# Kernel optimization log

Hardware: AMD Instinct MI355X
Metric: run time of the kernel (lower is better)

## Reference

```python
import jax, jax.numpy as jnp
import numpy as np


def setup_inputs() -> dict:
    key = jax.random.key(0)
    k0, k1, k2, k3 = jax.random.split(key, 4)
    B, S, D, F, E = 8, 2048, 1024, 2048, 8
    x = jax.random.normal(k0, (B, S, D), dtype=jnp.float32)
    Wg = jax.random.normal(k1, (D, E), dtype=jnp.float32) * 0.02
    W1 = jax.random.normal(k2, (E, D, F), dtype=jnp.float32) * 0.02
    W2 = jax.random.normal(k3, (E, F, D), dtype=jnp.float32) * 0.02
    return {"x": x, "Wg": Wg, "W1": W1, "W2": W2}


def reference(x, Wg, W1, W2):
    # Expert-choice MoE: experts pick top-C tokens, conflicts resolved by
    # max router prob (ties -> lowest expert index, matching the serial loop).
    B, S, D = x.shape
    E = Wg.shape[1]
    T = B * S
    cap = max(1, T // E)  # capacity_factor = 1.0

    xt = x.reshape(T, D)
    logits = xt @ Wg                      # [T, E]
    probs = jax.nn.softmax(logits, axis=-1)
    pT = probs.T                          # [E, T] token affinities per expert

    _, top_idx = jax.lax.top_k(pT, cap)   # [E, cap] tokens chosen by each expert
    sel = jnp.zeros((E, T), dtype=bool).at[jnp.arange(E)[:, None], top_idx].set(True)

    # Serial conflict loop is equivalent to: per token, pick the selecting
    masked = jnp.where(sel, pT, -jnp.inf)
    assigned = sel.any(axis=0)            # [T]
    tok2exp = jnp.where(assigned,
                        jnp.argmax(masked, axis=0),
                        jnp.argmax(pT, axis=0))          # [T] int
    weights = jnp.take_along_axis(probs, tok2exp[:, None], axis=1)[:, 0]  # [T]

    # Dispatch / expert FFN / weighted combine. Loop over the small fixed
    # expert set; masked tokens contribute exactly zero, matching index_add_.
    out = jnp.zeros_like(xt)
    for e in range(E):
        gate = jnp.where(tok2exp == e, weights, 0.0)     # [T]
        h = jax.nn.gelu(xt @ W1[e], approximate=False) @ W2[e]  # [T, D]
        out = out + gate[:, None] * h

    return out.reshape(B, S, D)
```

## Files before the change

kernel.cpp:

```cpp
#include <hip/hip_runtime.h>
#include <hip/hip_bf16.h>
#include <math.h>

#define T_TOK 16384
#define DIM   1024
#define FF    2048
#define NE    8
#define CAPK  2048
#define WL1SZ 4096
#define WL2SZ 2048
#define NB_W2T 4096

typedef unsigned short u16;
typedef unsigned long long u64;
typedef __attribute__((ext_vector_type(8))) short bf16x8;
typedef __attribute__((ext_vector_type(4))) float f32x4;

__device__ __forceinline__ u16 f2bf(float f) {
  __hip_bfloat16 h = __float2bfloat16(f);
  union { __hip_bfloat16 h; u16 u; } c; c.h = h; return c.u;
}

__device__ __forceinline__ float gelu_f(float v) {
  float z = fabsf(v) * 0.70710678118654752f;
  float t = __builtin_amdgcn_rcpf(1.0f + 0.3275911f * z);
  float poly = t * (0.254829592f +
               t * (-0.284496736f +
               t * (1.421413741f +
               t * (-1.453152027f +
               t * 1.061405429f))));
  float ez = __expf(-z * z);
  float erfz = 1.0f - poly * ez;
  erfz = copysignf(erfz, v);
  return 0.5f * v * (1.0f + erfz);
}

__device__ __forceinline__ void async_copy16(const void* g, void* l) {
  __builtin_amdgcn_global_load_lds(
      (const __attribute__((address_space(1))) unsigned int*)g,
      (__attribute__((address_space(3))) unsigned int*)l, 16, 0, 0);
}

__device__ __forceinline__ bf16x8 ds_read16(const char* p) {
  bf16x8 r;
  asm volatile("ds_read_b128 %0, %1"
               : "=&v"(r)
               : "v"((const __attribute__((address_space(3))) char*)p));
  return r;
}

#define LGKM0()                                                                   \
  do {                                                                            \
    asm volatile("s_waitcnt lgkmcnt(0)" ::: "memory");                            \
    __builtin_amdgcn_sched_barrier(0);                                            \
  } while (0)
#define VMW0() asm volatile("s_waitcnt vmcnt(0)" ::: "memory")
#define VMW4() asm volatile("s_waitcnt vmcnt(4)" ::: "memory")
#define BAR() asm volatile("s_barrier" ::: "memory")

__device__ __forceinline__ void transpose_tile(const float* __restrict__ src,
                                               u16* __restrict__ dst, int R, int C,
                                               int bxy, int tid, float (*tile)[65]) {
  int nbx = C >> 6;
  int bx = bxy % nbx, by = bxy / nbx;
  int r0 = by * 64, c0 = bx * 64;
  int lr = tid >> 4, lc4 = (tid & 15) * 4;
#pragma unroll
  for (int p = 0; p < 4; ++p) {
    float4 v = *(const float4*)(src + (size_t)(r0 + p * 16 + lr) * C + c0 + lc4);
    tile[p * 16 + lr][lc4 + 0] = v.x;
    tile[p * 16 + lr][lc4 + 1] = v.y;
    tile[p * 16 + lr][lc4 + 2] = v.z;
    tile[p * 16 + lr][lc4 + 3] = v.w;
  }
  __syncthreads();
  int oc = tid >> 3, orr = (tid & 7) * 8;
#pragma unroll
  for (int p = 0; p < 2; ++p) {
    int c = p * 32 + oc;
    u16 h[8];
#pragma unroll
    for (int j = 0; j < 8; ++j) h[j] = f2bf(tile[orr + j][c]);
    *(uint4*)(dst + (size_t)(c0 + c) * R + r0 + orr) = *(uint4*)h;
  }
}

__global__ __launch_bounds__(256) void prep_k(const float* __restrict__ x,
                                              const float* __restrict__ Wg,
                                              const float* __restrict__ W1,
                                              float* __restrict__ probs,
                                              float* __restrict__ probsT,
                                              u16* __restrict__ xb,
                                              u16* __restrict__ w1t,
                                              u64* __restrict__ key,
                                              int* cnt, int* cnt2, int* gates) {
  __shared__ float tile[64][65];
  int bid = blockIdx.x, tid = threadIdx.x;
  if (bid < 4096) {
    if (tid < 4) key[bid * 4 + tid] = 0ull;
    if (bid == 0 && tid < NE) { cnt[tid] = 0; cnt2[tid] = 0; }
    if (bid == 0 && tid >= 8 && tid < 10) gates[tid - 8] = 0;
    int wid = tid >> 6, lane = tid & 63;
    int t = bid * 4 + wid;
    const float* xr = x + (size_t)t * DIM;
    u16* xbr = xb + (size_t)t * DIM;
    double acc[NE] = {0, 0, 0, 0, 0, 0, 0, 0};
#pragma unroll
    for (int it = 0; it < DIM / 64; ++it) {
      int d = it * 64 + lane;
      float xv = xr[d];
      xbr[d] = f2bf(xv);
      const float4* wrow = (const float4*)(Wg + (size_t)d * NE);
      float4 w0 = wrow[0], w1 = wrow[1];
      acc[0] += (double)xv * (double)w0.x;
      acc[1] += (double)xv * (double)w0.y;
      acc[2] += (double)xv * (double)w0.z;
      acc[3] += (double)xv * (double)w0.w;
      acc[4] += (double)xv * (double)w1.x;
      acc[5] += (double)xv * (double)w1.y;
      acc[6] += (double)xv * (double)w1.z;
      acc[7] += (double)xv * (double)w1.w;
    }
#pragma unroll
    for (int e = 0; e < NE; ++e)
      for (int o = 32; o > 0; o >>= 1) acc[e] += __shfl_down(acc[e], o, 64);
    if (lane == 0) {
      float l[NE], mx = -3.0e38f;
#pragma unroll
      for (int e = 0; e < NE; ++e) { l[e] = (float)acc[e]; mx = fmaxf(mx, l[e]); }
      float s = 0.f;
#pragma unroll
      for (int e = 0; e < NE; ++e) { l[e] = expf(l[e] - mx); s += l[e]; }
      float inv = 1.0f / s;
#pragma unroll
      for (int e = 0; e < NE; ++e) {
        float p = l[e] * inv;
        probs[(size_t)t * NE + e] = p;
        probsT[(size_t)e * T_TOK + t] = p;
      }
    }
  } else {
    int tz = bid - 4096;
    int z = tz >> 9, bxy = tz & 511;
    transpose_tile(W1 + (size_t)z * DIM * FF, w1t + (size_t)z * DIM * FF,
                   DIM, FF, bxy, tid, tile);
  }
}

__global__ __launch_bounds__(256) void moe_route_k(const float* __restrict__ probsT,
                                                   const float* __restrict__ probs,
                                                   const float* __restrict__ W2,
                                                   u16* __restrict__ w2t,
                                                   u64* __restrict__ key,
                                                   int* __restrict__ tok2exp,
                                                   float* __restrict__ wgt,
                                                   int* cnt, int* cnt2,
                                                   int* __restrict__ list,
                                                   int* basep, int* wl1, int* wl2,
                                                   int* gates) {
  __shared__ char shm[17472];
  int bid = blockIdx.x, tid = threadIdx.x, wid = tid >> 6, lane = tid & 63;
  if (bid < 8) {
    unsigned* whist = (unsigned*)shm;
    unsigned* hist  = (unsigned*)(shm + 16384);
    unsigned* bcast = (unsigned*)(shm + 17408);
    unsigned* wsum  = (unsigned*)(shm + 17424);
    int*      wps   = (int*)(shm + 17440);
    int e = bid;
    const float* pT = probsT + (size_t)e * T_TOK;
    unsigned prefix = 0, remaining = CAPK;
#pragma unroll 1
    for (int lvl = 0; lvl < 4; ++lvl) {
      int shift = 24 - 8 * lvl;
      unsigned cv;
      if (lvl == 0) {
        for (int i = tid; i < 16 * 256; i += 256) whist[i] = 0;
        __syncthreads();
        int sub = wid * 4 + (lane & 3);
        for (int i = tid; i < T_TOK; i += 256)
          atomicAdd(&whist[sub * 256 + (__float_as_uint(pT[i]) >> 24)], 1u);
        __syncthreads();
        cv = 0;
#pragma unroll
        for (int w = 0; w < 16; ++w) cv += whist[w * 256 + tid];
      } else {
        hist[tid] = 0;
        __syncthreads();
        for (int i = tid; i < T_TOK; i += 256) {
          unsigned k = __float_as_uint(pT[i]);
          if ((k >> (shift + 8)) == prefix)
            atomicAdd(&hist[(k >> shift) & 255u], 1u);
        }
        __syncthreads();
        cv = hist[tid];
      }
      unsigned s = cv;
#pragma unroll
      for (int o = 1; o < 64; o <<= 1) {
        unsigned tv = __shfl_down(s, o, 64);
        if (lane + o < 64) s += tv;
      }
      if (lane == 0) wsum[wid] = s;
      __syncthreads();
      unsigned above = 0;
      for (int w = wid + 1; w < 4; ++w) above += wsum[w];
      unsigned Sincl = s + above, Sexcl = Sincl - cv;
      if (Sincl >= remaining && Sexcl < remaining) {
        bcast[0] = (unsigned)tid;
        bcast[1] = remaining - Sexcl;
      }
      __syncthreads();
      prefix = (prefix << 8) | bcast[0];
      remaining = bcast[1];
      __syncthreads();
    }
    unsigned vk = prefix;
    int need = (int)remaining;
    const int CH = T_TOK / 256;
    int i0 = tid * CH;
    int myt = 0;
    for (int i = i0; i < i0 + CH; ++i)
      myt += (__float_as_uint(pT[i]) == vk);
    int p = myt;
#pragma unroll
    for (int o = 1; o < 64; o <<= 1) {
      int tv = __shfl_up(p, o, 64);
      if (lane >= o) p += tv;
    }
    if (lane == 63) wps[wid] = p;
    __syncthreads();
    int wo = 0;
    for (int w = 0; w < wid; ++w) wo += wps[w];
    int run = wo + p - myt;
    u64 ebits = (u64)(7 - e);
    for (int i = i0; i < i0 + CH; ++i) {
      unsigned k = __float_as_uint(pT[i]);
      bool sv = false;
      if (k > vk) sv = true;
      else if (k == vk) { if (run < need) sv = true; run++; }
      if (sv) atomicMax(&key[i], ((u64)k << 3) | ebits);
    }
    __threadfence();
    __syncthreads();
    if (tid == 0) atomicAdd(&gates[0], 1);
  } else if (bid < 72) {
    if (tid == 0) {
      while (atomicAdd(&gates[0], 0) < 8) __builtin_amdgcn_s_sleep(8);
    }
    __syncthreads();
    __threadfence();
    int gid = (bid - 8) * 256 + tid;
    u64 k = key[gid];
    int best;
    float bp;
    if (k) {
      best = 7 - (int)(k & 7);
      bp = __uint_as_float((unsigned)(k >> 3));
    } else {
      best = 0; bp = -3.0e38f;
#pragma unroll
      for (int e = 0; e < NE; ++e) {
        float p = probs[(size_t)gid * NE + e];
        if (p > bp) { bp = p; best = e; }
      }
    }
    tok2exp[gid] = best;
    wgt[gid] = bp;
#pragma unroll
    for (int e = 0; e < NE; ++e) {
      u64 m = __ballot(best == e);
      if (best == e && lane == __ffsll(m) - 1) atomicAdd(&cnt[e], (int)__popcll(m));
    }
    __threadfence();
    __syncthreads();
    if (tid == 0) atomicAdd(&gates[1], 1);
    if (tid == 0) {
      while (atomicAdd(&gates[1], 0) < 64) __builtin_amdgcn_s_sleep(8);
    }
    __syncthreads();
    __threadfence();
    int c[NE];
#pragma unroll
    for (int e = 0; e < NE; ++e) c[e] = cnt[e];
    if (gid < NE) {
      int r = 0;
      for (int e = 0; e < gid; ++e) r += c[e];
      basep[gid] = r;
    }
    if (gid < WL1SZ) {
      int e = gid & 7, j = gid >> 3;
      int mte = (c[e] + 255) >> 8;
      wl1[gid] = (j < mte * 8) ? (e | ((j >> 3) << 4) | ((j & 7) << 12)) : -1;
    }
    if (gid >= WL1SZ && gid < WL1SZ + WL2SZ) {
      int g2 = gid - WL1SZ;
      int e = g2 & 7, j = g2 >> 3;
      int mte = (c[e] + 255) >> 8;
      wl2[g2] = (j < mte * 4) ? (e | ((j >> 2) << 4) | ((j & 3) << 12)) : -1;
    }
    int te = tok2exp[gid];
    int bp_e = 0;
#pragma unroll
    for (int e = 0; e < NE; ++e) if (e < te) bp_e += c[e];
    int sl = 0;
#pragma unroll
    for (int e = 0; e < NE; ++e) {
      u64 m = __ballot(te == e);
      if (te == e) {
        int leader = __ffsll(m) - 1;
        int rank = __popcll(m & ((1ull << lane) - 1));
        int b = 0;
        if (lane == leader) b = atomicAdd(&cnt2[e], (int)__popcll(m));
        b = __shfl(b, leader, 64);
        sl = bp_e + b + rank;
      }
    }
    list[sl] = gid;
  } else {
    int tz = bid - 72;
    int z = tz >> 9, bxy = tz & 511;
    transpose_tile(W2 + (size_t)z * FF * DIM, w2t + (size_t)z * FF * DIM,
                   FF, DIM, bxy, tid, (float (*)[65])shm);
  }
}


#define MM2(M, N_, AK0, AK1, BK0, BK1)                                            \
  acc[M][N_] = __builtin_amdgcn_mfma_f32_16x16x32_bf16(BK0, AK0, acc[M][N_], 0, 0, 0); \
  acc[M][N_] = __builtin_amdgcn_mfma_f32_16x16x32_bf16(BK1, AK1, acc[M][N_], 0, 0, 0);

#define MFMA_Q(MH, NH, B00, B01, B10, B11)                                        \
  do {                                                                            \
    __builtin_amdgcn_s_setprio(1);                                                \
    MM2((MH)*4+0, (NH)*2+0, a0k0, a0k1, B00, B01);                                \
    MM2((MH)*4+0, (NH)*2+1, a0k0, a0k1, B10, B11);                                \
    MM2((MH)*4+1, (NH)*2+0, a1k0, a1k1, B00, B01);                                \
    MM2((MH)*4+1, (NH)*2+1, a1k0, a1k1, B10, B11);                                \
    MM2((MH)*4+2, (NH)*2+0, a2k0, a2k1, B00, B01);                                \
    MM2((MH)*4+2, (NH)*2+1, a2k0, a2k1, B10, B11);                                \
    MM2((MH)*4+3, (NH)*2+0, a3k0, a3k1, B00, B01);                                \
    MM2((MH)*4+3, (NH)*2+1, a3k0, a3k1, B10, B11);                                \
    __builtin_amdgcn_s_setprio(0);                                                \
  } while (0)

#define RD_A(d, mh)                                                               \
  do {                                                                            \
    const char* p = sm + (d) * 65536 + wr * 16384 + (mh) * 4096 + laneOff;        \
    a0k0 = ds_read16(p);         a1k0 = ds_read16(p + 1024);                      \
    a2k0 = ds_read16(p + 2048);  a3k0 = ds_read16(p + 3072);                      \
    a0k1 = ds_read16(p + 8192);  a1k1 = ds_read16(p + 9216);                      \
    a2k1 = ds_read16(p + 10240); a3k1 = ds_read16(p + 11264);                     \
  } while (0)

#define RD_B(d, nh, B00, B01, B10, B11)                                           \
  do {                                                                            \
    const char* p = sm + (d) * 65536 + 32768 + (wc >> 1) * 16384 +                \
                    (wc & 1) * 4096 + (nh) * 2048 + laneOff;                      \
    B00 = ds_read16(p);        B10 = ds_read16(p + 1024);                         \
    B01 = ds_read16(p + 8192); B11 = ds_read16(p + 9216);                         \
  } while (0)

#define STG(P, regoff, t)                                                         \
  do {                                                                            \
    char* dst = sm + (((t) & 1) * 65536) + (regoff) + tid * 16;                   \
    const char* s = (P) + (size_t)(t) * 128;                                      \
    async_copy16(s, dst);                                                         \
    async_copy16(s + 64, dst + 8192);                                             \
  } while (0)

template <int EPI>
__global__ __launch_bounds__(512, 2) void ffn_k(const u16* __restrict__ A,
                                                const u16* __restrict__ Bm,
                                                void* __restrict__ Out,
                                                const int* __restrict__ list,
                                                const float* __restrict__ wgt,
                                                const int* __restrict__ basep,
                                                const int* __restrict__ cnt,
                                                const int* __restrict__ wl) {
  constexpr int K = EPI ? FF : DIM;
  constexpr int N = EPI ? DIM : FF;
  constexpr int KT = K / 64;

  const int wle = wl[blockIdx.x];
  if (wle < 0) return;
  const int e = wle & 15, mt = (wle >> 4) & 255, nt = wle >> 12;
  const int ce = cnt[e];
  const int be = basep[e];

  __shared__ u16 smem[65536];
  __shared__ int toks[256];
  __shared__ float wsc[256];
  char* const sm = (char*)smem;
  const int tid = threadIdx.x;

  if (tid < 256) {
    int r = mt * 256 + tid;
    int tk = (r < ce) ? list[be + r] : list[be];
    toks[tid] = tk;
    if (EPI == 1) wsc[tid] = wgt[tk];
  }
  __syncthreads();

  const int wid = tid >> 6, lane = tid & 63;
  const int wr = wid >> 2, wc = wid & 3;
  const int laneOff = ((lane & 15) >> 1) * 128 + (lane & 1) * 64 +
                      (((lane >> 4) << 4) ^ ((((lane & 15) >> 1) & 3) << 4));

  const int r0 = 2 * (tid >> 3) + ((tid & 7) >> 2);
  const int cbl = ((tid & 3) << 4) ^ (((tid >> 3) & 3) << 4);
  const char *aH0P, *aH1P;
  if (EPI == 0) {
    aH0P = (const char*)(A + (size_t)toks[r0] * K) + cbl;
    aH1P = (const char*)(A + (size_t)toks[128 + r0] * K) + cbl;
  } else {
    aH0P = (const char*)(A + ((size_t)be + mt * 256 + r0) * K) + cbl;
    aH1P = (const char*)(A + ((size_t)be + mt * 256 + 128 + r0) * K) + cbl;
  }
  const char* bH0P = (const char*)(Bm + ((size_t)e * N + nt * 256 + r0) * K) + cbl;
  const char* bH1P = (const char*)(Bm + ((size_t)e * N + nt * 256 + 128 + r0) * K) + cbl;

  f32x4 acc[8][4];
#pragma unroll
  for (int m = 0; m < 8; ++m)
#pragma unroll
    for (int n = 0; n < 4; ++n) acc[m][n] = (f32x4){0.f, 0.f, 0.f, 0.f};

  bf16x8 a0k0, a0k1, a1k0, a1k1, a2k0, a2k1, a3k0, a3k1;
  bf16x8 b00, b01, b10, b11;
  bf16x8 c00, c01, c10, c11;

  STG(bH0P, 32768, 0); STG(bH1P, 49152, 0);
  STG(aH0P, 0, 0);     STG(aH1P, 16384, 0);
  STG(bH0P, 32768, 1); STG(bH1P, 49152, 1);
  VMW0();
  BAR();

#pragma unroll 1
  for (int t = 0; t < KT; ++t) {
    const int d = t & 1;
    RD_A(d, 0);
    RD_B(d, 0, b00, b01, b10, b11);
    if (t + 1 < KT) STG(aH0P, 0, t + 1);
    BAR(); LGKM0();
    MFMA_Q(0, 0, b00, b01, b10, b11);
    BAR();
    RD_B(d, 1, c00, c01, c10, c11);
    if (t + 1 < KT) STG(aH1P, 16384, t + 1);
    BAR(); LGKM0();
    MFMA_Q(0, 1, c00, c01, c10, c11);
    BAR();
    RD_A(d, 1);
    if (t + 2 < KT) STG(bH0P, 32768, t + 2);
    BAR(); LGKM0();
    MFMA_Q(1, 1, c00, c01, c10, c11);
    BAR();
    if (t + 2 < KT) STG(bH1P, 49152, t + 2);
    if (t < KT - 2) { VMW4(); } else { VMW0(); }
    BAR(); LGKM0();
    MFMA_Q(1, 0, b00, b01, b10, b11);
    BAR();
  }

  const int lc = lane & 15, lq = (lane >> 4) * 4;
#pragma unroll
  for (int m = 0; m < 8; ++m) {
    int trow = wr * 128 + m * 16 + lc;
    int grow = mt * 256 + trow;
    if (grow < ce) {
      if (EPI == 0) {
        size_t rowoff = (size_t)(be + grow) * FF + nt * 256 + wc * 64 + lq;
#pragma unroll
        for (int n = 0; n < 4; ++n) {
          ushort4 h4;
          h4.x = f2bf(gelu_f(acc[m][n][0]));
          h4.y = f2bf(gelu_f(acc[m][n][1]));
          h4.z = f2bf(gelu_f(acc[m][n][2]));
          h4.w = f2bf(gelu_f(acc[m][n][3]));
          *(ushort4*)((u16*)Out + rowoff + n * 16) = h4;
        }
      } else {
        float w = wsc[trow];
        size_t rowoff = (size_t)toks[trow] * DIM + nt * 256 + wc * 64 + lq;
#pragma unroll
        for (int n = 0; n < 4; ++n) {
          float4 o = make_float4(w * acc[m][n][0], w * acc[m][n][1],
                                 w * acc[m][n][2], w * acc[m][n][3]);
          *(float4*)((float*)Out + rowoff + n * 16) = o;
        }
      }
    }
  }
}

extern "C" void kernel_launch(void* const* d_in, const int* in_sizes, int n_in,
                              void* d_out, int out_size, void* d_ws, size_t ws_size,
                              hipStream_t stream) {
  (void)in_sizes; (void)n_in; (void)out_size; (void)ws_size;
  const float* x  = (const float*)d_in[0];
  const float* Wg = (const float*)d_in[1];
  const float* W1 = (const float*)d_in[2];
  const float* W2 = (const float*)d_in[3];
  float* out = (float*)d_out;

  char* ws = (char*)d_ws;
  size_t off = 0;
  auto alloc = [&](size_t bytes) -> void* {
    void* p = ws + off;
    off += (bytes + 255) & ~(size_t)255;
    return p;
  };
  u16* xb   = (u16*)alloc((size_t)T_TOK * DIM * 2);
  u16* w1t  = (u16*)alloc((size_t)NE * FF * DIM * 2);
  u16* w2t  = (u16*)alloc((size_t)NE * DIM * FF * 2);
  u16* H    = (u16*)alloc((size_t)(T_TOK + 256) * FF * 2);
  float* probs  = (float*)alloc((size_t)T_TOK * NE * 4);
  float* probsT = (float*)alloc((size_t)NE * T_TOK * 4);
  u64* key      = (u64*)alloc((size_t)T_TOK * 8);
  float* wgt    = (float*)alloc((size_t)T_TOK * 4);
  int* tok2exp  = (int*)alloc((size_t)T_TOK * 4);
  int* list     = (int*)alloc((size_t)T_TOK * 4);
  int* cnt      = (int*)alloc(64);
  int* cnt2     = (int*)alloc(64);
  int* basep    = (int*)alloc(64);
  int* gates    = (int*)alloc(64);
  int* wl1      = (int*)alloc(WL1SZ * 4);
  int* wl2      = (int*)alloc(WL2SZ * 4);

  prep_k<<<4096 + 4096, 256, 0, stream>>>(x, Wg, W1, probs, probsT, xb, w1t,
                                          key, cnt, cnt2, gates);
  moe_route_k<<<72 + NB_W2T, 256, 0, stream>>>(probsT, probs, W2, w2t, key,
                                               tok2exp, wgt, cnt, cnt2,
                                               list, basep, wl1, wl2, gates);
  ffn_k<0><<<WL1SZ, 512, 0, stream>>>(xb, w1t, H, list, wgt, basep, cnt, wl1);
  ffn_k<1><<<WL2SZ, 512, 0, stream>>>(H, w2t, out, list, wgt, basep, cnt, wl2);
}
```

Before: 433.8 us.

## Move W2 transpose into prep kernel and stage router column in LDS with 3-level radix select

After: 398.6 us. 1.09x faster.

```diff
diff --git a/kernel.cpp b/kernel.cpp
--- a/kernel.cpp
+++ b/kernel.cpp
@@ -9,7 +9,6 @@
 #define CAPK  2048
 #define WL1SZ 4096
 #define WL2SZ 2048
-#define NB_W2T 4096
 
 typedef unsigned short u16;
 typedef unsigned long long u64;
@@ -88,10 +87,12 @@
 __global__ __launch_bounds__(256) void prep_k(const float* __restrict__ x,
                                               const float* __restrict__ Wg,
                                               const float* __restrict__ W1,
+                                              const float* __restrict__ W2,
                                               float* __restrict__ probs,
                                               float* __restrict__ probsT,
                                               u16* __restrict__ xb,
                                               u16* __restrict__ w1t,
+                                              u16* __restrict__ w2t,
                                               u64* __restrict__ key,
                                               int* cnt, int* cnt2, int* gates) {
   __shared__ float tile[64][65];
@@ -142,15 +143,17 @@
   } else {
     int tz = bid - 4096;
     int z = tz >> 9, bxy = tz & 511;
-    transpose_tile(W1 + (size_t)z * DIM * FF, w1t + (size_t)z * DIM * FF,
-                   DIM, FF, bxy, tid, tile);
+    if (z < 8)
+      transpose_tile(W1 + (size_t)z * DIM * FF, w1t + (size_t)z * DIM * FF,
+                     DIM, FF, bxy, tid, tile);
+    else
+      transpose_tile(W2 + (size_t)(z - 8) * FF * DIM, w2t + (size_t)(z - 8) * FF * DIM,
+                     FF, DIM, bxy, tid, tile);
   }
 }
 
 __global__ __launch_bounds__(256) void moe_route_k(const float* __restrict__ probsT,
                                                    const float* __restrict__ probs,
-                                                   const float* __restrict__ W2,
-                                                   u16* __restrict__ w2t,
                                                    u64* __restrict__ key,
                                                    int* __restrict__ tok2exp,
                                                    float* __restrict__ wgt,
@@ -158,42 +161,47 @@
                                                    int* __restrict__ list,
                                                    int* basep, int* wl1, int* wl2,
                                                    int* gates) {
-  __shared__ char shm[17472];
+  __shared__ float pcol[T_TOK];
+  __shared__ unsigned whist[8][2048];
+  __shared__ unsigned hist[2048];
+  __shared__ unsigned bcast[2];
+  __shared__ unsigned wsum[4];
+  __shared__ int wps[4];
   int bid = blockIdx.x, tid = threadIdx.x, wid = tid >> 6, lane = tid & 63;
   if (bid < 8) {
-    unsigned* whist = (unsigned*)shm;
-    unsigned* hist  = (unsigned*)(shm + 16384);
-    unsigned* bcast = (unsigned*)(shm + 17408);
-    unsigned* wsum  = (unsigned*)(shm + 17424);
-    int*      wps   = (int*)(shm + 17440);
     int e = bid;
-    const float* pT = probsT + (size_t)e * T_TOK;
+    const float4* src4 = (const float4*)(probsT + (size_t)e * T_TOK);
+    for (int i = tid; i < T_TOK / 4; i += 256) ((float4*)pcol)[i] = src4[i];
+    for (int i = tid; i < 8 * 2048; i += 256) ((unsigned*)whist)[i] = 0;
     unsigned prefix = 0, remaining = CAPK;
 #pragma unroll 1
-    for (int lvl = 0; lvl < 4; ++lvl) {
-      int shift = 24 - 8 * lvl;
-      unsigned cv;
+    for (int lvl = 0; lvl < 3; ++lvl) {
+      int nb = (lvl == 2) ? 1024 : 2048;
       if (lvl == 0) {
-        for (int i = tid; i < 16 * 256; i += 256) whist[i] = 0;
         __syncthreads();
-        int sub = wid * 4 + (lane & 3);
         for (int i = tid; i < T_TOK; i += 256)
-          atomicAdd(&whist[sub * 256 + (__float_as_uint(pT[i]) >> 24)], 1u);
+          atomicAdd(&whist[wid][__float_as_uint(pcol[i]) >> 21], 1u);
         __syncthreads();
-        cv = 0;
-#pragma unroll
-        for (int w = 0; w < 16; ++w) cv += whist[w * 256 + tid];
+        for (int j = tid; j < 2048; j += 256) {
+          unsigned s2 = 0;
+#pragma unroll
+          for (int w = 0; w < 8; ++w) s2 += whist[w][j];
+          hist[j] = s2;
+        }
+        __syncthreads();
       } else {
-        hist[tid] = 0;
+        for (int i = tid; i < 2048; i += 256) hist[i] = 0;
         __syncthreads();
         for (int i = tid; i < T_TOK; i += 256) {
-          unsigned k = __float_as_uint(pT[i]);
-          if ((k >> (shift + 8)) == prefix)
-            atomicAdd(&hist[(k >> shift) & 255u], 1u);
+          unsigned k = __float_as_uint(pcol[i]);
+          bool m = (lvl == 1) ? ((k >> 21) == prefix) : ((k >> 10) == prefix);
+          if (m) atomicAdd(&hist[(lvl == 1) ? ((k >> 10) & 2047u) : (k & 1023u)], 1u);
         }
         __syncthreads();
-        cv = hist[tid];
-      }
+      }
+      int nper = nb / 256;
+      unsigned cv = 0;
+      for (int j = 0; j < nper; ++j) cv += hist[tid * nper + j];
       unsigned s = cv;
 #pragma unroll
       for (int o = 1; o < 64; o <<= 1) {
@@ -206,12 +214,17 @@
       for (int w = wid + 1; w < 4; ++w) above += wsum[w];
       unsigned Sincl = s + above, Sexcl = Sincl - cv;
       if (Sincl >= remaining && Sexcl < remaining) {
-        bcast[0] = (unsigned)tid;
-        bcast[1] = remaining - Sexcl;
+        unsigned rem2 = remaining - Sexcl, cum2 = 0;
+        for (int j = nper - 1; j >= 0; --j) {
+          unsigned h = hist[tid * nper + j];
+          if (cum2 + h >= rem2) { bcast[0] = (unsigned)(tid * nper + j); bcast[1] = rem2 - cum2; break; }
+          cum2 += h;
+        }
       }
       __syncthreads();
-      prefix = (prefix << 8) | bcast[0];
+      unsigned b = bcast[0];
       remaining = bcast[1];
+      prefix = (lvl == 0) ? b : (lvl == 1) ? ((prefix << 11) | b) : ((prefix << 10) | b);
       __syncthreads();
     }
     unsigned vk = prefix;
@@ -220,7 +233,7 @@
     int i0 = tid * CH;
     int myt = 0;
     for (int i = i0; i < i0 + CH; ++i)
-      myt += (__float_as_uint(pT[i]) == vk);
+      myt += (__float_as_uint(pcol[i]) == vk);
     int p = myt;
 #pragma unroll
     for (int o = 1; o < 64; o <<= 1) {
@@ -234,7 +247,7 @@
     int run = wo + p - myt;
     u64 ebits = (u64)(7 - e);
     for (int i = i0; i < i0 + CH; ++i) {
-      unsigned k = __float_as_uint(pT[i]);
+      unsigned k = __float_as_uint(pcol[i]);
       bool sv = false;
       if (k > vk) sv = true;
       else if (k == vk) { if (run < need) sv = true; run++; }
@@ -243,7 +256,7 @@
     __threadfence();
     __syncthreads();
     if (tid == 0) atomicAdd(&gates[0], 1);
-  } else if (bid < 72) {
+  } else {
     if (tid == 0) {
       while (atomicAdd(&gates[0], 0) < 8) __builtin_amdgcn_s_sleep(8);
     }
@@ -316,11 +329,6 @@
       }
     }
     list[sl] = gid;
-  } else {
-    int tz = bid - 72;
-    int z = tz >> 9, bxy = tz & 511;
-    transpose_tile(W2 + (size_t)z * FF * DIM, w2t + (size_t)z * FF * DIM,
-                   FF, DIM, bxy, tid, (float (*)[65])shm);
   }
 }
 
@@ -526,11 +534,10 @@
   int* wl1      = (int*)alloc(WL1SZ * 4);
   int* wl2      = (int*)alloc(WL2SZ * 4);
 
-  prep_k<<<4096 + 4096, 256, 0, stream>>>(x, Wg, W1, probs, probsT, xb, w1t,
+  prep_k<<<4096 + 8192, 256, 0, stream>>>(x, Wg, W1, W2, probs, probsT, xb, w1t, w2t,
                                           key, cnt, cnt2, gates);
-  moe_route_k<<<72 + NB_W2T, 256, 0, stream>>>(probsT, probs, W2, w2t, key,
-                                               tok2exp, wgt, cnt, cnt2,
-                                               list, basep, wl1, wl2, gates);
+  moe_route_k<<<72, 256, 0, stream>>>(probsT, probs, key, tok2exp, wgt, cnt, cnt2,
+                                      list, basep, wl1, wl2, gates);
   ffn_k<0><<<WL1SZ, 512, 0, stream>>>(xb, w1t, H, list, wgt, basep, cnt, wl1);
   ffn_k<1><<<WL2SZ, 512, 0, stream>>>(H, w2t, out, list, wgt, basep, cnt, wl2);
 }
```
